# Optimization experiments

Hardware: AMD Instinct MI355X
Metric: run time of the kernel (lower is better)

Reference implementation:

```python
import math
import jax, jax.numpy as jnp
import numpy as np

B, S, D, H = 4, 2048, 768, 12
HD = D // H  # 64


def setup_inputs() -> dict:
    key = jax.random.key(0)
    ks = jax.random.split(key, 10)
    sc = 0.02
    return {
        "hidden_states": jax.random.normal(ks[0], (B, S, D), dtype=jnp.float32),
        "attention_mask": jax.random.randint(ks[1], (1, H, S, S), 0, 2).astype(jnp.bool_),
        "q_w": jax.random.normal(ks[2], (D, D), dtype=jnp.float32) * sc,
        "q_b": jax.random.normal(ks[3], (D,), dtype=jnp.float32) * sc,
        "k_w": jax.random.normal(ks[4], (D, D), dtype=jnp.float32) * sc,
        "k_b": jax.random.normal(ks[5], (D,), dtype=jnp.float32) * sc,
        "v_w": jax.random.normal(ks[6], (D, D), dtype=jnp.float32) * sc,
        "v_b": jax.random.normal(ks[7], (D,), dtype=jnp.float32) * sc,
        "out_w": jax.random.normal(ks[8], (D, D), dtype=jnp.float32) * sc,
        "out_b": jax.random.normal(ks[9], (D,), dtype=jnp.float32) * sc,
    }


def _split_heads(x):
    # [B, S, D] -> [B, H, S, HD]
    b, s, _ = x.shape
    return x.reshape(b, s, H, HD).transpose(0, 2, 1, 3)


def reference(hidden_states, attention_mask, q_w, q_b, k_w, k_b, v_w, v_b, out_w, out_b):
    q = _split_heads(hidden_states @ q_w.T + q_b)
    k = _split_heads(hidden_states @ k_w.T + k_b)
    v = _split_heads(hidden_states @ v_w.T + v_b)
    scores = jnp.einsum("bhqd,bhkd->bhqk", q, k) / math.sqrt(HD)
    # prune_mode, before softmax: masked_fill(~mask, -inf)
    scores = jnp.where(attention_mask, scores, -jnp.inf)
    probs = jax.nn.softmax(scores, axis=-1)  # [B, H, S, S]
    ctx = jnp.einsum("bhqk,bhkd->bhqd", probs, v)
    ctx = ctx.transpose(0, 2, 1, 3).reshape(hidden_states.shape[0], -1, D)
    return ctx @ out_w.T + out_b
```

## Files before the change

kernel.cpp:

```cpp
#include <hip/hip_runtime.h>
#include <hip/hip_bf16.h>

#define B_ 4
#define S_ 2048
#define D_ 768
#define H_ 12
#define HD_ 64

typedef __attribute__((ext_vector_type(8))) short bf16x8;
typedef __attribute__((ext_vector_type(4))) float floatx4;

#define QSCALE 0.18033688011112042f

__device__ __forceinline__ unsigned short f2bf(float x) {
    union { float f; unsigned int u; } v; v.f = x;
    unsigned int r = v.u + 0x7fffu + ((v.u >> 16) & 1u);
    return (unsigned short)(r >> 16);
}

__device__ __forceinline__ void gload_lds16(const void* g, void* l) {
    __builtin_amdgcn_global_load_lds(
        (const __attribute__((address_space(1))) unsigned int*)g,
        (__attribute__((address_space(3))) unsigned int*)l, 16, 0, 0);
}

__device__ __forceinline__ bf16x8 ld_b64x2(const unsigned short* p) {
    union { bf16x8 v; unsigned long long q[2]; } u;
    u.q[0] = *(const unsigned long long*)p;
    u.q[1] = *(const unsigned long long*)(p + 4);
    return u.v;
}

__global__ void cast_f32_bf16(const float* __restrict__ src,
                              unsigned short* __restrict__ dst, int n4) {
    int i = blockIdx.x * 256 + threadIdx.x;
    if (i >= n4) return;
    float4 f = ((const float4*)src)[i];
    ushort4 o;
    o.x = f2bf(f.x); o.y = f2bf(f.y); o.z = f2bf(f.z); o.w = f2bf(f.w);
    ((ushort4*)dst)[i] = o;
}

__global__ void cast_w4(const float* __restrict__ w0, const float* __restrict__ w1,
                        const float* __restrict__ w2, const float* __restrict__ w3,
                        unsigned short* __restrict__ dst, int n4 ) {
    const float* src = (blockIdx.y == 0) ? w0 : (blockIdx.y == 1) ? w1
                     : (blockIdx.y == 2) ? w2 : w3;
    unsigned short* d = dst + (size_t)blockIdx.y * (size_t)n4 * 4;
    int i = blockIdx.x * 256 + threadIdx.x;
    if (i >= n4) return;
    float4 f = ((const float4*)src)[i];
    ushort4 o;
    o.x = f2bf(f.x); o.y = f2bf(f.y); o.z = f2bf(f.z); o.w = f2bf(f.w);
    ((ushort4*)d)[i] = o;
}

__global__ void pack_mask(const int* __restrict__ mask,
                          unsigned long long* __restrict__ bits) {
    size_t gw = (size_t)(blockIdx.x * 256 + threadIdx.x) >> 6;
    int lane = threadIdx.x & 63;
    size_t base = gw * 256;
    unsigned long long b0 = __ballot(mask[base + lane] != 0);
    unsigned long long b1 = __ballot(mask[base + 64 + lane] != 0);
    unsigned long long b2 = __ballot(mask[base + 128 + lane] != 0);
    unsigned long long b3 = __ballot(mask[base + 192 + lane] != 0);
    if (lane == 0) {
        bits[gw * 4 + 0] = b0; bits[gw * 4 + 1] = b1;
        bits[gw * 4 + 2] = b2; bits[gw * 4 + 3] = b3;
    }
}

__global__ __launch_bounds__(256) void qkv_gemm(
    const unsigned short* __restrict__ Xb,
    const unsigned short* __restrict__ Wq, const unsigned short* __restrict__ Wk,
    const unsigned short* __restrict__ Wv,
    const float* __restrict__ bq, const float* __restrict__ bk,
    const float* __restrict__ bv,
    unsigned short* __restrict__ Qo, unsigned short* __restrict__ Ko,
    unsigned short* __restrict__ Vo)
{
    const int z = blockIdx.z;
    const unsigned short* W = (z == 0) ? Wq : (z == 1) ? Wk : Wv;
    const float* bias = (z == 0) ? bq : (z == 1) ? bk : bv;
    unsigned short* Out = (z == 0) ? Qo : (z == 1) ? Ko : Vo;
    const float scale = (z == 0) ? QSCALE : 1.0f;

    const int m0 = blockIdx.x * 128;
    const int n0 = blockIdx.y * 128;

    __shared__ alignas(16) unsigned short As[128 * 32];
    __shared__ alignas(16) unsigned short Bs[128 * 32];

    const int t = threadIdx.x;
    const int lane = t & 63, w = t >> 6;
    const int c = lane & 15, quad = lane >> 4;
    const int wm = (w & 1) * 64, wn = (w >> 1) * 64;

    floatx4 acc[4][4];
#pragma unroll
    for (int i = 0; i < 4; i++)
#pragma unroll
        for (int j = 0; j < 4; j++) acc[i][j] = (floatx4){0.f, 0.f, 0.f, 0.f};

    for (int k0 = 0; k0 < 768; k0 += 32) {
#pragma unroll
        for (int i = 0; i < 2; i++) {
            int chunk = i * 4 + w;
            int row = chunk * 16 + (lane >> 2);
            int col8 = (lane & 3) * 8;
            gload_lds16(&Xb[(size_t)(m0 + row) * 768 + k0 + col8], &As[chunk * 512]);
            gload_lds16(&W [(size_t)(n0 + row) * 768 + k0 + col8], &Bs[chunk * 512]);
        }
        __syncthreads();
        bf16x8 a[4], b[4];
#pragma unroll
        for (int i = 0; i < 4; i++)
            a[i] = *(const bf16x8*)&As[(wm + i * 16 + c) * 32 + quad * 8];
#pragma unroll
        for (int j = 0; j < 4; j++)
            b[j] = *(const bf16x8*)&Bs[(wn + j * 16 + c) * 32 + quad * 8];
#pragma unroll
        for (int i = 0; i < 4; i++)
#pragma unroll
            for (int j = 0; j < 4; j++)
                acc[i][j] = __builtin_amdgcn_mfma_f32_16x16x32_bf16(
                    a[i], b[j], acc[i][j], 0, 0, 0);
        __syncthreads();
    }

    if (z == 2) {
#pragma unroll
        for (int i = 0; i < 4; i++) {
#pragma unroll
            for (int j = 0; j < 4; j++) {
                int nn = n0 + wn + j * 16 + c;
                float bias_n = bias[nn];
                int hh = nn >> 6, dd = nn & 63;
#pragma unroll
                for (int r = 0; r < 4; r++) {
                    int mm = m0 + wm + i * 16 + quad * 4 + r;
                    int bb = mm >> 11, ss = mm & 2047;
                    float v = acc[i][j][r] + bias_n;
                    Out[(((size_t)(bb * H_ + hh)) * 64 + dd) * S_ + ss] = f2bf(v);
                }
            }
        }
    } else {
#pragma unroll
        for (int i = 0; i < 4; i++) {
#pragma unroll
            for (int j = 0; j < 4; j++) {
                int nn = n0 + wn + j * 16 + c;
                float bias_n = bias[nn];
                int hh = nn >> 6, dd = nn & 63;
#pragma unroll
                for (int r = 0; r < 4; r++) {
                    int mm = m0 + wm + i * 16 + quad * 4 + r;
                    int bb = mm >> 11, ss = mm & 2047;
                    float v = (acc[i][j][r] + bias_n) * scale;
                    Out[(((size_t)(bb * H_ + hh)) * S_ + ss) * 64 + dd] = f2bf(v);
                }
            }
        }
    }
}

__global__ __launch_bounds__(256) void out_gemm(
    const unsigned short* __restrict__ Cb, const unsigned short* __restrict__ Wo,
    const float* __restrict__ bo, float* __restrict__ out)
{
    const int m0 = blockIdx.x * 128;
    const int n0 = blockIdx.y * 128;

    __shared__ alignas(16) unsigned short As[128 * 32];
    __shared__ alignas(16) unsigned short Bs[128 * 32];

    const int t = threadIdx.x;
    const int lane = t & 63, w = t >> 6;
    const int c = lane & 15, quad = lane >> 4;
    const int wm = (w & 1) * 64, wn = (w >> 1) * 64;

    floatx4 acc[4][4];
#pragma unroll
    for (int i = 0; i < 4; i++)
#pragma unroll
        for (int j = 0; j < 4; j++) acc[i][j] = (floatx4){0.f, 0.f, 0.f, 0.f};

    for (int k0 = 0; k0 < 768; k0 += 32) {
#pragma unroll
        for (int i = 0; i < 2; i++) {
            int chunk = i * 4 + w;
            int row = chunk * 16 + (lane >> 2);
            int col8 = (lane & 3) * 8;
            gload_lds16(&Cb[(size_t)(m0 + row) * 768 + k0 + col8], &As[chunk * 512]);
            gload_lds16(&Wo[(size_t)(n0 + row) * 768 + k0 + col8], &Bs[chunk * 512]);
        }
        __syncthreads();
        bf16x8 a[4], b[4];
#pragma unroll
        for (int i = 0; i < 4; i++)
            a[i] = *(const bf16x8*)&As[(wm + i * 16 + c) * 32 + quad * 8];
#pragma unroll
        for (int j = 0; j < 4; j++)
            b[j] = *(const bf16x8*)&Bs[(wn + j * 16 + c) * 32 + quad * 8];
#pragma unroll
        for (int i = 0; i < 4; i++)
#pragma unroll
            for (int j = 0; j < 4; j++)
                acc[i][j] = __builtin_amdgcn_mfma_f32_16x16x32_bf16(
                    a[i], b[j], acc[i][j], 0, 0, 0);
        __syncthreads();
    }

#pragma unroll
    for (int i = 0; i < 4; i++) {
#pragma unroll
        for (int j = 0; j < 4; j++) {
            int nn = n0 + wn + j * 16 + c;
            float bias_n = bo[nn];
#pragma unroll
            for (int r = 0; r < 4; r++) {
                int mm = m0 + wm + i * 16 + quad * 4 + r;
                out[(size_t)mm * 768 + nn] = acc[i][j][r] + bias_n;
            }
        }
    }
}

__global__ __launch_bounds__(256) void attn(
    const unsigned short* __restrict__ Q, const unsigned short* __restrict__ K,
    const unsigned short* __restrict__ Vt,
    const unsigned long long* __restrict__ mbits,
    unsigned short* __restrict__ ctx)
{
    const int qt = blockIdx.x;
    const int bh = blockIdx.y;
    const int b = bh / H_, h = bh % H_;

    const unsigned short* Qp = Q + (size_t)bh * S_ * 64 + (size_t)qt * 64 * 64;
    const unsigned short* Kp = K + (size_t)bh * S_ * 64;
    const unsigned short* Vp = Vt + (size_t)bh * 64 * S_;

    __shared__ alignas(16) unsigned short Ks[2][64 * 64];
    __shared__ alignas(16) unsigned short Vs[2][64 * 64];
    __shared__ alignas(16) unsigned short Ps[4][16 * 68];

    const int t = threadIdx.x;
    const int lane = t & 63, w = t >> 6;
    const int c = lane & 15, quad = lane >> 4;

    bf16x8 aq0 = *(const bf16x8*)&Qp[(size_t)(w * 16 + c) * 64 + quad * 8];
    bf16x8 aq1 = *(const bf16x8*)&Qp[(size_t)(w * 16 + c) * 64 + 32 + quad * 8];

    const unsigned long long* mrow =
        mbits + ((size_t)h * S_ + qt * 64 + w * 16 + quad * 4) * (S_ / 64);

    floatx4 acc_o[4];
#pragma unroll
    for (int i = 0; i < 4; i++) acc_o[i] = (floatx4){0.f, 0.f, 0.f, 0.f};
    float lp[4] = {0.f, 0.f, 0.f, 0.f};

    const int ldK = lane >> 3, lcK = (lane & 7) * 8;

#pragma unroll
    for (int i = 0; i < 2; i++) {
        int chunk = i * 4 + w;
        gload_lds16(&Kp[(size_t)(chunk * 8 + ldK) * 64 + lcK], &Ks[0][chunk * 512]);
        gload_lds16(&Vp[(size_t)(chunk * 8 + ldK) * S_ + lcK], &Vs[0][chunk * 512]);
    }

    for (int kt = 0; kt < S_ / 64; kt++) {
        const int cur = kt & 1;
        __syncthreads();
        if (kt + 1 < S_ / 64) {
#pragma unroll
            for (int i = 0; i < 2; i++) {
                int chunk = i * 4 + w;
                gload_lds16(&Kp[(size_t)((kt + 1) * 64 + chunk * 8 + ldK) * 64 + lcK],
                            &Ks[cur ^ 1][chunk * 512]);
                gload_lds16(&Vp[(size_t)(chunk * 8 + ldK) * S_ + (kt + 1) * 64 + lcK],
                            &Vs[cur ^ 1][chunk * 512]);
            }
        }

        floatx4 sacc[4];
#pragma unroll
        for (int nt = 0; nt < 4; nt++) {
            bf16x8 bk0 = *(const bf16x8*)&Ks[cur][(nt * 16 + c) * 64 + quad * 8];
            bf16x8 bk1 = *(const bf16x8*)&Ks[cur][(nt * 16 + c) * 64 + 32 + quad * 8];
            floatx4 zz = (floatx4){0.f, 0.f, 0.f, 0.f};
            zz = __builtin_amdgcn_mfma_f32_16x16x32_bf16(aq0, bk0, zz, 0, 0, 0);
            zz = __builtin_amdgcn_mfma_f32_16x16x32_bf16(aq1, bk1, zz, 0, 0, 0);
            sacc[nt] = zz;
        }

#pragma unroll
        for (int r = 0; r < 4; r++) {
            unsigned long long M = mrow[r * (S_ / 64) + kt];
            unsigned int lo = (unsigned int)M, hi = (unsigned int)(M >> 32);
            float p0 = ((lo >> c) & 1)        ? __builtin_amdgcn_exp2f(sacc[0][r]) : 0.f;
            float p1 = ((lo >> (c + 16)) & 1) ? __builtin_amdgcn_exp2f(sacc[1][r]) : 0.f;
            float p2 = ((hi >> c) & 1)        ? __builtin_amdgcn_exp2f(sacc[2][r]) : 0.f;
            float p3 = ((hi >> (c + 16)) & 1) ? __builtin_amdgcn_exp2f(sacc[3][r]) : 0.f;
            lp[r] += (p0 + p1) + (p2 + p3);
            int row = quad * 4 + r;
            Ps[w][row * 68 +      c] = f2bf(p0);
            Ps[w][row * 68 + 16 + c] = f2bf(p1);
            Ps[w][row * 68 + 32 + c] = f2bf(p2);
            Ps[w][row * 68 + 48 + c] = f2bf(p3);
        }
        asm volatile("" ::: "memory");

        bf16x8 ap0 = ld_b64x2(&Ps[w][c * 68 + quad * 8]);
        bf16x8 ap1 = ld_b64x2(&Ps[w][c * 68 + 32 + quad * 8]);
#pragma unroll
        for (int nt = 0; nt < 4; nt++) {
            bf16x8 bv0 = *(const bf16x8*)&Vs[cur][(nt * 16 + c) * 64 + quad * 8];
            bf16x8 bv1 = *(const bf16x8*)&Vs[cur][(nt * 16 + c) * 64 + 32 + quad * 8];
            acc_o[nt] = __builtin_amdgcn_mfma_f32_16x16x32_bf16(ap0, bv0, acc_o[nt], 0, 0, 0);
            acc_o[nt] = __builtin_amdgcn_mfma_f32_16x16x32_bf16(ap1, bv1, acc_o[nt], 0, 0, 0);
        }
    }

#pragma unroll
    for (int r = 0; r < 4; r++) {
        float s = lp[r];
#pragma unroll
        for (int o = 1; o < 16; o <<= 1) s += __shfl_xor(s, o, 64);
        lp[r] = s;
    }

#pragma unroll
    for (int nt = 0; nt < 4; nt++) {
#pragma unroll
        for (int r = 0; r < 4; r++) {
            int qrow = qt * 64 + w * 16 + quad * 4 + r;
            int dd = nt * 16 + c;
            float v = acc_o[nt][r] / lp[r];
            ctx[((size_t)b * S_ + qrow) * 768 + h * 64 + dd] = f2bf(v);
        }
    }
}

extern "C" void kernel_launch(void* const* d_in, const int* in_sizes, int n_in,
                              void* d_out, int out_size, void* d_ws, size_t ws_size,
                              hipStream_t stream) {
    const float* hs    = (const float*)d_in[0];
    const int*   mask  = (const int*)d_in[1];
    const float* q_w   = (const float*)d_in[2];
    const float* q_b   = (const float*)d_in[3];
    const float* k_w   = (const float*)d_in[4];
    const float* k_b   = (const float*)d_in[5];
    const float* v_w   = (const float*)d_in[6];
    const float* v_b   = (const float*)d_in[7];
    const float* out_w = (const float*)d_in[8];
    const float* out_b = (const float*)d_in[9];
    float* out = (float*)d_out;

    unsigned short* Xb  = (unsigned short*)d_ws;
    unsigned short* Wqb = Xb + 6291456;
    unsigned short* Wkb = Wqb + 589824;
    unsigned short* Wvb = Wkb + 589824;
    unsigned short* Wob = Wvb + 589824;
    unsigned short* Qb  = Wob + 589824;
    unsigned short* Kb  = Qb + 6291456;
    unsigned short* Vtb = Kb + 6291456;
    unsigned short* Cb  = Vtb + 6291456;
    unsigned long long* mbits = (unsigned long long*)(Cb + 6291456);

    cast_f32_bf16<<<6144, 256, 0, stream>>>(hs, Xb, 1572864);
    cast_w4<<<dim3(576, 4), 256, 0, stream>>>(q_w, k_w, v_w, out_w, Wqb, 147456);
    pack_mask<<<49152, 256, 0, stream>>>(mask, mbits);
    qkv_gemm<<<dim3(64, 6, 3), 256, 0, stream>>>(Xb, Wqb, Wkb, Wvb,
                                                 q_b, k_b, v_b, Qb, Kb, Vtb);
    attn<<<dim3(32, 48), 256, 0, stream>>>(Qb, Kb, Vtb, mbits, Cb);
    out_gemm<<<dim3(64, 6), 256, 0, stream>>>(Cb, Wob, out_b, out);
}
```

Baseline: 528.0 us.

## Swizzle K/V LDS tiles, permute key columns for packed P stores, coalesce V-transpose stores

The attention kernel now loads K and V tiles into LDS with an XOR column swizzle and reads them back with matching swizzled offsets. This is meant to remove LDS bank conflicts on the MFMA operand loads. Key and head-dim columns are remapped to 4*c+nt, so each lane extracts a single 4-bit mask nibble and writes its four probabilities as one packed 64-bit bf16 store. The QKV GEMM now stages the transposed V output through swizzled shared memory so global writes go out as 16-byte coalesced rows instead of scattered 2-byte stores. The cost is two extra barriers in that epilogue and more delicate index math that must stay consistent with the mask bit layout.

```diff
diff --git a/kernel.cpp b/kernel.cpp
--- a/kernel.cpp
+++ b/kernel.cpp
@@ -16,6 +16,13 @@
     union { float f; unsigned int u; } v; v.f = x;
     unsigned int r = v.u + 0x7fffu + ((v.u >> 16) & 1u);
     return (unsigned short)(r >> 16);
+}
+
+__device__ __forceinline__ unsigned int pk2bf(float a, float b) {
+    __hip_bfloat162 h = __float22bfloat162_rn(make_float2(a, b));
+    unsigned int u;
+    __builtin_memcpy(&u, &h, 4);
+    return u;
 }
 
 __device__ __forceinline__ void gload_lds16(const void* g, void* l) {
@@ -88,8 +95,9 @@
     const int m0 = blockIdx.x * 128;
     const int n0 = blockIdx.y * 128;
 
-    __shared__ alignas(16) unsigned short As[128 * 32];
-    __shared__ alignas(16) unsigned short Bs[128 * 32];
+    __shared__ alignas(16) unsigned short SM[8192];
+    unsigned short* As = SM;
+    unsigned short* Bs = SM + 4096;
 
     const int t = threadIdx.x;
     const int lane = t & 63, w = t >> 6;
@@ -107,9 +115,9 @@
         for (int i = 0; i < 2; i++) {
             int chunk = i * 4 + w;
             int row = chunk * 16 + (lane >> 2);
-            int col8 = (lane & 3) * 8;
-            gload_lds16(&Xb[(size_t)(m0 + row) * 768 + k0 + col8], &As[chunk * 512]);
-            gload_lds16(&W [(size_t)(n0 + row) * 768 + k0 + col8], &Bs[chunk * 512]);
+            int c8 = (lane & 3) * 8;
+            gload_lds16(&Xb[(size_t)(m0 + row) * 768 + k0 + c8], &As[chunk * 512]);
+            gload_lds16(&W [(size_t)(n0 + row) * 768 + k0 + c8], &Bs[chunk * 512]);
         }
         __syncthreads();
         bf16x8 a[4], b[4];
@@ -129,21 +137,42 @@
     }
 
     if (z == 2) {
-#pragma unroll
-        for (int i = 0; i < 4; i++) {
-#pragma unroll
-            for (int j = 0; j < 4; j++) {
-                int nn = n0 + wn + j * 16 + c;
-                float bias_n = bias[nn];
-                int hh = nn >> 6, dd = nn & 63;
-#pragma unroll
-                for (int r = 0; r < 4; r++) {
-                    int mm = m0 + wm + i * 16 + quad * 4 + r;
-                    int bb = mm >> 11, ss = mm & 2047;
-                    float v = acc[i][j][r] + bias_n;
-                    Out[(((size_t)(bb * H_ + hh)) * 64 + dd) * S_ + ss] = f2bf(v);
+        const int bb = m0 >> 11, ssb = m0 & 2047;
+#pragma unroll
+        for (int half = 0; half < 2; half++) {
+            if ((w >> 1) == half) {
+#pragma unroll
+                for (int j = 0; j < 4; j++) {
+                    int n_l = j * 16 + c;
+                    float bias_n = bias[n0 + half * 64 + n_l];
+#pragma unroll
+                    for (int i = 0; i < 4; i++) {
+#pragma unroll
+                        for (int r = 0; r < 4; r++) {
+                            int m = wm + i * 16 + quad * 4 + r;
+                            int ms = m ^ (c << 3);
+                            SM[n_l * 128 + ms] = f2bf(acc[i][j][r] + bias_n);
+                        }
+                    }
                 }
             }
+            __syncthreads();
+#pragma unroll
+            for (int rb = 0; rb < 2; rb++) {
+                int n_l = (t >> 3) + rb * 32;
+                int ch = t & 7;
+                int n_abs = n0 + half * 64 + n_l;
+                int hh = n_abs >> 6, dd = n_abs & 63;
+                unsigned short* dst =
+                    Out + (((size_t)(bb * H_ + hh)) * 64 + dd) * S_ + ssb;
+#pragma unroll
+                for (int p = 0; p < 2; p++) {
+                    int mc = ch + p * 8;
+                    uint4 v = *(const uint4*)&SM[n_l * 128 + ((mc ^ (n_l & 15)) * 8)];
+                    *(uint4*)&dst[mc * 8] = v;
+                }
+            }
+            __syncthreads();
         }
     } else {
 #pragma unroll
@@ -191,9 +220,9 @@
         for (int i = 0; i < 2; i++) {
             int chunk = i * 4 + w;
             int row = chunk * 16 + (lane >> 2);
-            int col8 = (lane & 3) * 8;
-            gload_lds16(&Cb[(size_t)(m0 + row) * 768 + k0 + col8], &As[chunk * 512]);
-            gload_lds16(&Wo[(size_t)(n0 + row) * 768 + k0 + col8], &Bs[chunk * 512]);
+            int c8 = (lane & 3) * 8;
+            gload_lds16(&Cb[(size_t)(m0 + row) * 768 + k0 + c8], &As[chunk * 512]);
+            gload_lds16(&Wo[(size_t)(n0 + row) * 768 + k0 + c8], &Bs[chunk * 512]);
         }
         __syncthreads();
         bf16x8 a[4], b[4];
@@ -260,13 +289,17 @@
     for (int i = 0; i < 4; i++) acc_o[i] = (floatx4){0.f, 0.f, 0.f, 0.f};
     float lp[4] = {0.f, 0.f, 0.f, 0.f};
 
-    const int ldK = lane >> 3, lcK = (lane & 7) * 8;
+    const int srow = (lane >> 3);
+    const int rc0 = ((quad     ) ^ (c & 7)) * 8;
+    const int rc1 = ((quad + 4) ^ (c & 7)) * 8;
 
 #pragma unroll
     for (int i = 0; i < 2; i++) {
         int chunk = i * 4 + w;
-        gload_lds16(&Kp[(size_t)(chunk * 8 + ldK) * 64 + lcK], &Ks[0][chunk * 512]);
-        gload_lds16(&Vp[(size_t)(chunk * 8 + ldK) * S_ + lcK], &Vs[0][chunk * 512]);
+        int row = chunk * 8 + srow;
+        int col8 = (((lane & 7) ^ ((row >> 2) & 7))) * 8;
+        gload_lds16(&Kp[(size_t)row * 64 + col8], &Ks[0][chunk * 512]);
+        gload_lds16(&Vp[(size_t)row * S_ + col8], &Vs[0][chunk * 512]);
     }
 
     for (int kt = 0; kt < S_ / 64; kt++) {
@@ -276,9 +309,11 @@
 #pragma unroll
             for (int i = 0; i < 2; i++) {
                 int chunk = i * 4 + w;
-                gload_lds16(&Kp[(size_t)((kt + 1) * 64 + chunk * 8 + ldK) * 64 + lcK],
+                int row = chunk * 8 + srow;
+                int col8 = (((lane & 7) ^ ((row >> 2) & 7))) * 8;
+                gload_lds16(&Kp[(size_t)((kt + 1) * 64 + row) * 64 + col8],
                             &Ks[cur ^ 1][chunk * 512]);
-                gload_lds16(&Vp[(size_t)(chunk * 8 + ldK) * S_ + (kt + 1) * 64 + lcK],
+                gload_lds16(&Vp[(size_t)row * S_ + (kt + 1) * 64 + col8],
                             &Vs[cur ^ 1][chunk * 512]);
             }
         }
@@ -286,8 +321,9 @@
         floatx4 sacc[4];
 #pragma unroll
         for (int nt = 0; nt < 4; nt++) {
-            bf16x8 bk0 = *(const bf16x8*)&Ks[cur][(nt * 16 + c) * 64 + quad * 8];
-            bf16x8 bk1 = *(const bf16x8*)&Ks[cur][(nt * 16 + c) * 64 + 32 + quad * 8];
+            int kr = 4 * c + nt;
+            bf16x8 bk0 = *(const bf16x8*)&Ks[cur][kr * 64 + rc0];
+            bf16x8 bk1 = *(const bf16x8*)&Ks[cur][kr * 64 + rc1];
             floatx4 zz = (floatx4){0.f, 0.f, 0.f, 0.f};
             zz = __builtin_amdgcn_mfma_f32_16x16x32_bf16(aq0, bk0, zz, 0, 0, 0);
             zz = __builtin_amdgcn_mfma_f32_16x16x32_bf16(aq1, bk1, zz, 0, 0, 0);
@@ -296,18 +332,16 @@
 
 #pragma unroll
         for (int r = 0; r < 4; r++) {
-            unsigned long long M = mrow[r * (S_ / 64) + kt];
-            unsigned int lo = (unsigned int)M, hi = (unsigned int)(M >> 32);
-            float p0 = ((lo >> c) & 1)        ? __builtin_amdgcn_exp2f(sacc[0][r]) : 0.f;
-            float p1 = ((lo >> (c + 16)) & 1) ? __builtin_amdgcn_exp2f(sacc[1][r]) : 0.f;
-            float p2 = ((hi >> c) & 1)        ? __builtin_amdgcn_exp2f(sacc[2][r]) : 0.f;
-            float p3 = ((hi >> (c + 16)) & 1) ? __builtin_amdgcn_exp2f(sacc[3][r]) : 0.f;
+            unsigned int nib = (unsigned int)(mrow[r * (S_ / 64) + kt] >> (4 * c)) & 15u;
+            float p0 = (nib & 1u) ? __builtin_amdgcn_exp2f(sacc[0][r]) : 0.f;
+            float p1 = (nib & 2u) ? __builtin_amdgcn_exp2f(sacc[1][r]) : 0.f;
+            float p2 = (nib & 4u) ? __builtin_amdgcn_exp2f(sacc[2][r]) : 0.f;
+            float p3 = (nib & 8u) ? __builtin_amdgcn_exp2f(sacc[3][r]) : 0.f;
             lp[r] += (p0 + p1) + (p2 + p3);
-            int row = quad * 4 + r;
-            Ps[w][row * 68 +      c] = f2bf(p0);
-            Ps[w][row * 68 + 16 + c] = f2bf(p1);
-            Ps[w][row * 68 + 32 + c] = f2bf(p2);
-            Ps[w][row * 68 + 48 + c] = f2bf(p3);
+            unsigned long long pk =
+                (unsigned long long)pk2bf(p0, p1) |
+                ((unsigned long long)pk2bf(p2, p3) << 32);
+            *(unsigned long long*)&Ps[w][(quad * 4 + r) * 68 + 4 * c] = pk;
         }
         asm volatile("" ::: "memory");
 
@@ -315,8 +349,9 @@
         bf16x8 ap1 = ld_b64x2(&Ps[w][c * 68 + 32 + quad * 8]);
 #pragma unroll
         for (int nt = 0; nt < 4; nt++) {
-            bf16x8 bv0 = *(const bf16x8*)&Vs[cur][(nt * 16 + c) * 64 + quad * 8];
-            bf16x8 bv1 = *(const bf16x8*)&Vs[cur][(nt * 16 + c) * 64 + 32 + quad * 8];
+            int vr = 4 * c + nt;
+            bf16x8 bv0 = *(const bf16x8*)&Vs[cur][vr * 64 + rc0];
+            bf16x8 bv1 = *(const bf16x8*)&Vs[cur][vr * 64 + rc1];
             acc_o[nt] = __builtin_amdgcn_mfma_f32_16x16x32_bf16(ap0, bv0, acc_o[nt], 0, 0, 0);
             acc_o[nt] = __builtin_amdgcn_mfma_f32_16x16x32_bf16(ap1, bv1, acc_o[nt], 0, 0, 0);
         }
@@ -335,7 +370,7 @@
 #pragma unroll
         for (int r = 0; r < 4; r++) {
             int qrow = qt * 64 + w * 16 + quad * 4 + r;
-            int dd = nt * 16 + c;
+            int dd = 4 * c + nt;
             float v = acc_o[nt][r] / lp[r];
             ctx[((size_t)b * S_ + qrow) * 768 + h * 64 + dd] = f2bf(v);
         }
```

Result: faster. 508.1 us (-3.8%).
